# Performance work log

Hardware: AMD Instinct MI355X
Metric: run time of the kernel (lower is better)

The kernel has to match this reference:

```python
import jax, jax.numpy as jnp
import numpy as np

N = 100000
E = 1600000
IN_FEATS = 128
HID = 128


def _xavier(key, shape):
    fan_in, fan_out = shape[0], shape[1]
    limit = float(np.sqrt(6.0 / (fan_in + fan_out)))
    return jax.random.uniform(key, shape, jnp.float32, -limit, limit)


def setup_inputs() -> dict:
    key = jax.random.key(0)
    ks = jax.random.split(key, 10)
    x = jax.random.normal(ks[0], (N, IN_FEATS), jnp.float32)
    edge_index = jax.random.randint(ks[1], (2, E), 0, N, jnp.int64)
    inp = {"x": x, "edge_index": edge_index}
    # GCNConv weights (stored as [in, out] so h = x @ W)
    inp["W1"] = _xavier(ks[2], (IN_FEATS, HID)); inp["b1"] = jnp.zeros((HID,), jnp.float32)
    inp["W2"] = _xavier(ks[3], (HID, HID));      inp["b2"] = jnp.zeros((HID,), jnp.float32)
    inp["W3"] = _xavier(ks[4], (HID, HID));      inp["b3"] = jnp.zeros((HID,), jnp.float32)
    # position head: Linear(HID,HID) -> ReLU -> Linear(HID,2)
    inp["Wp1"] = _xavier(ks[5], (HID, HID)); inp["bp1"] = jnp.zeros((HID,), jnp.float32)
    inp["Wp2"] = _xavier(ks[6], (HID, 2));   inp["bp2"] = jnp.zeros((2,), jnp.float32)
    # time head: Linear(HID,HID//2) -> ReLU -> Linear(HID//2,1)
    inp["Wt1"] = _xavier(ks[7], (HID, HID // 2)); inp["bt1"] = jnp.zeros((HID // 2,), jnp.float32)
    inp["Wt2"] = _xavier(ks[8], (HID // 2, 1));   inp["bt2"] = jnp.zeros((1,), jnp.float32)
    return inp


def _gcn_conv(x, src, dst, norm, W, b):
    # PyG GCNConv: out = D^{-1/2} (A + I) D^{-1/2} (x W) + b
    h = x @ W                                  # [N, out]
    msg = h[src] * norm[:, None]               # gather over edges (+ self-loops)
    agg = jax.ops.segment_sum(msg, dst, num_segments=N)  # scatter-add to dst
    return agg + b


def reference(x, edge_index, W1, b1, W2, b2, W3, b3, Wp1, bp1, Wp2, bp2, Wt1, bt1, Wt2, bt2):
    src, dst = edge_index[0], edge_index[1]
    # add self-loops once (shared across the 3 conv layers)
    loop = jnp.arange(N, dtype=edge_index.dtype)
    src_a = jnp.concatenate([src, loop])
    dst_a = jnp.concatenate([dst, loop])
    # symmetric normalization: deg computed on dst (in-degree incl. self-loop)
    deg = jax.ops.segment_sum(jnp.ones_like(dst_a, dtype=x.dtype), dst_a, num_segments=N)
    dinv = jnp.where(deg > 0, jax.lax.rsqrt(deg), 0.0)
    norm = dinv[src_a] * dinv[dst_a]           # [E + N]

    h = jax.nn.relu(_gcn_conv(x, src_a, dst_a, norm, W1, b1))
    h = jax.nn.relu(_gcn_conv(h, src_a, dst_a, norm, W2, b2))
    h = jax.nn.relu(_gcn_conv(h, src_a, dst_a, norm, W3, b3))

    pos = jax.nn.relu(h @ Wp1 + bp1) @ Wp2 + bp2     # [N, 2]
    time = jax.nn.relu(h @ Wt1 + bt1) @ Wt2 + bt2    # [N, 1]
    return jnp.concatenate([pos, time], axis=1)      # [N, 3]
```

## Files before the change

kernel.cpp:

```cpp
#include <hip/hip_runtime.h>

typedef __bf16 bf16x8 __attribute__((ext_vector_type(8)));
typedef unsigned short u16x8 __attribute__((ext_vector_type(8)));
typedef float f32x4 __attribute__((ext_vector_type(4)));

union BU {
    u16x8 u;
    bf16x8 b;
};

static __device__ __forceinline__ float b2f(unsigned short u) {
    return __uint_as_float(((unsigned)u) << 16);
}
static __device__ __forceinline__ unsigned short f2b(float f) {
    unsigned u = __float_as_uint(f);
    unsigned r = (u + 0x7FFF + ((u >> 16) & 1)) >> 16;
    return (unsigned short)r;
}

__global__ __launch_bounds__(256) void wsplit_kernel(
    const float* __restrict__ W1, const float* __restrict__ W2, const float* __restrict__ W3,
    const float* __restrict__ Wp1, const float* __restrict__ Wt1,
    unsigned short* __restrict__ W1hi, unsigned short* __restrict__ W1lo,
    unsigned short* __restrict__ W2hi, unsigned short* __restrict__ W2lo,
    unsigned short* __restrict__ W3hi, unsigned short* __restrict__ W3lo,
    unsigned short* __restrict__ Wchi, unsigned short* __restrict__ Wclo,
    const float* __restrict__ bp1, const float* __restrict__ bt1, float* __restrict__ bcat) {
    int b = blockIdx.x;
    int tid = threadIdx.x;
    if (b < 288) {
        const float* W;
        unsigned short *Whi, *Wlo;
        int lb, ncshift, total;
        if (b < 64)       { W = W1;  Whi = W1hi; Wlo = W1lo; lb = b;       ncshift = 7; total = 16384; }
        else if (b < 128) { W = W2;  Whi = W2hi; Wlo = W2lo; lb = b - 64;  ncshift = 7; total = 16384; }
        else if (b < 192) { W = W3;  Whi = W3hi; Wlo = W3lo; lb = b - 128; ncshift = 7; total = 16384; }
        else if (b < 256) { W = Wp1; Whi = Wchi; Wlo = Wclo; lb = b - 192; ncshift = 7; total = 16384; }
        else              { W = Wt1; Whi = Wchi + 128 * 128; Wlo = Wclo + 128 * 128; lb = b - 256; ncshift = 6; total = 8192; }
        int idx = lb * 256 + tid;
        if (idx < total) {
            int k = idx >> ncshift;
            int n = idx - (k << ncshift);
            float a = W[idx];
            unsigned short hb = f2b(a);
            Whi[(n << 7) + k] = hb;
            Wlo[(n << 7) + k] = f2b(a - b2f(hb));
        }
        return;
    }
    if (tid < 128) bcat[tid] = bp1[tid];
    else if (tid < 192) bcat[tid] = bt1[tid - 128];
}

static __device__ __forceinline__ void split8(const float4 a01, const float4 a23,
                                              bf16x8& hi, bf16x8& lo) {
    float a[8] = {a01.x, a01.y, a01.z, a01.w, a23.x, a23.y, a23.z, a23.w};
    BU h, l;
#pragma unroll
    for (int j = 0; j < 8; ++j) {
        unsigned short hb = f2b(a[j]);
        h.u[j] = hb;
        l.u[j] = f2b(a[j] - b2f(hb));
    }
    hi = h.b;
    lo = l.b;
}

template <int NT>
static __device__ __forceinline__ void gemm_acc_f32(const float* __restrict__ A,
                                                    const unsigned short* __restrict__ Whi,
                                                    const unsigned short* __restrict__ Wlo,
                                                    int arow, int m16, int quad, f32x4* acc) {
    const float* Arow = A + (size_t)arow * 128 + quad * 8;
#pragma unroll
    for (int kb = 0; kb < 4; ++kb) {
        float4 a01 = *reinterpret_cast<const float4*>(Arow + kb * 32);
        float4 a23 = *reinterpret_cast<const float4*>(Arow + kb * 32 + 4);
        bf16x8 ahi, alo;
        split8(a01, a23, ahi, alo);
#pragma unroll
        for (int t = 0; t < NT; ++t) {
            size_t woff = (size_t)(t * 16 + m16) * 128 + quad * 8 + kb * 32;
            BU bh, bl;
            bh.u = *reinterpret_cast<const u16x8*>(Whi + woff);
            bl.u = *reinterpret_cast<const u16x8*>(Wlo + woff);
            acc[t] = __builtin_amdgcn_mfma_f32_16x16x32_bf16(ahi, bh.b, acc[t], 0, 0, 0);
            acc[t] = __builtin_amdgcn_mfma_f32_16x16x32_bf16(ahi, bl.b, acc[t], 0, 0, 0);
            acc[t] = __builtin_amdgcn_mfma_f32_16x16x32_bf16(alo, bh.b, acc[t], 0, 0, 0);
        }
    }
}

template <int NT>
static __device__ __forceinline__ void gemm_acc(const unsigned short* __restrict__ A,
                                                const unsigned short* __restrict__ Whi,
                                                const unsigned short* __restrict__ Wlo,
                                                int arow, int m16, int quad, f32x4* acc) {
    const unsigned short* Arow = A + (size_t)arow * 128 + quad * 8;
#pragma unroll
    for (int kb = 0; kb < 4; ++kb) {
        BU a;
        a.u = *reinterpret_cast<const u16x8*>(Arow + kb * 32);
#pragma unroll
        for (int t = 0; t < NT; ++t) {
            size_t woff = (size_t)(t * 16 + m16) * 128 + quad * 8 + kb * 32;
            BU bh, bl;
            bh.u = *reinterpret_cast<const u16x8*>(Whi + woff);
            bl.u = *reinterpret_cast<const u16x8*>(Wlo + woff);
            acc[t] = __builtin_amdgcn_mfma_f32_16x16x32_bf16(a.b, bh.b, acc[t], 0, 0, 0);
            acc[t] = __builtin_amdgcn_mfma_f32_16x16x32_bf16(a.b, bl.b, acc[t], 0, 0, 0);
        }
    }
}

template <int NT>
static __device__ __forceinline__ void gemm_store_plain(unsigned short* __restrict__ C,
                                                        int row_base, int m16, int quad,
                                                        f32x4* acc, int nrows) {
#pragma unroll
    for (int t = 0; t < NT; ++t) {
#pragma unroll
        for (int r = 0; r < 4; ++r) {
            int row = row_base + quad * 4 + r;
            if (row < nrows)
                C[(size_t)row * (NT * 16) + t * 16 + m16] = f2b(acc[t][r]);
        }
    }
}

template <int NT>
static __device__ __forceinline__ void gemm_store_scaled(const int* __restrict__ deg,
                                                         unsigned short* __restrict__ C,
                                                         int row_base, int m16, int quad,
                                                         f32x4* acc, int nrows) {
#pragma unroll
    for (int t = 0; t < NT; ++t) {
#pragma unroll
        for (int r = 0; r < 4; ++r) {
            int row = row_base + quad * 4 + r;
            if (row < nrows) {
                float d = rsqrtf((float)deg[row] + 1.0f);
                C[(size_t)row * (NT * 16) + t * 16 + m16] = f2b(acc[t][r] * d);
            }
        }
    }
}

__global__ __launch_bounds__(256) void fg2_kernel(const float* __restrict__ A,
                                                  const unsigned short* __restrict__ Whi,
                                                  const unsigned short* __restrict__ Wlo,
                                                  unsigned short* __restrict__ C, int nrows,
                                                  int fbn,
                                                  const int* __restrict__ ei,
                                                  int* __restrict__ deg,
                                                  int* __restrict__ slots, int E) {
    const int bid = blockIdx.x;
    const int tid = threadIdx.x;
    const int trip = bid / 3, r = bid % 3;
    if (r == 1 && trip < fbn) {
        int base = (trip * 256 + tid) * 8;
        int dsts[8], srcs[8], ps[8];
#pragma unroll
        for (int k = 0; k < 8; ++k) {
            int e = base + k;
            dsts[k] = (e < E) ? ei[E + e] : -1;
            srcs[k] = (e < E) ? ei[e] : 0;
        }
#pragma unroll
        for (int k = 0; k < 8; ++k)
            if (dsts[k] >= 0) ps[k] = atomicAdd(&deg[dsts[k]], 1);
#pragma unroll
        for (int k = 0; k < 8; ++k)
            if (dsts[k] >= 0 && ps[k] < 64)
                __builtin_nontemporal_store(srcs[k], &slots[(size_t)dsts[k] * 64 + ps[k]]);
    } else {
        int gid = bid - min(trip, fbn) - ((r > 1 && trip < fbn) ? 1 : 0);
        const int wave = tid >> 6, lane = tid & 63;
        const int m16 = lane & 15, quad = lane >> 4;
        const int row_base = gid * 64 + wave * 16;
        int arow = row_base + m16;
        if (arow >= nrows) arow = nrows - 1;
        f32x4 acc[8] = {};
        gemm_acc_f32<8>(A, Whi, Wlo, arow, m16, quad, acc);
        gemm_store_plain<8>(C, row_base, m16, quad, acc, nrows);
    }
}

__global__ __launch_bounds__(256) void scale_kernel(unsigned short* __restrict__ hs,
                                                    const int* __restrict__ deg, int n) {
    int idx = blockIdx.x * 256 + threadIdx.x;
    int node = idx >> 5;
    if (node >= n) return;
    int f = (idx & 31) * 4;
    float d = rsqrtf((float)deg[node] + 1.0f);
    ushort4 v = *reinterpret_cast<const ushort4*>(hs + (size_t)node * 128 + f);
    ushort4 o;
    o.x = f2b(b2f(v.x) * d);
    o.y = f2b(b2f(v.y) * d);
    o.z = f2b(b2f(v.z) * d);
    o.w = f2b(b2f(v.w) * d);
    *reinterpret_cast<ushort4*>(hs + (size_t)node * 128 + f) = o;
}

template <int NT>
__global__ __launch_bounds__(256) void gemm_kernel(const unsigned short* __restrict__ A,
                                                   const unsigned short* __restrict__ Whi,
                                                   const unsigned short* __restrict__ Wlo,
                                                   const int* __restrict__ deg,
                                                   unsigned short* __restrict__ C, int nrows) {
    const int tid = threadIdx.x;
    const int wave = tid >> 6, lane = tid & 63;
    const int m16 = lane & 15, quad = lane >> 4;
    const int row_base = blockIdx.x * 64 + wave * 16;
    int arow = row_base + m16;
    if (arow >= nrows) arow = nrows - 1;
    f32x4 acc[NT] = {};
    gemm_acc<NT>(A, Whi, Wlo, arow, m16, quad, acc);
    gemm_store_scaled<NT>(deg, C, row_base, m16, quad, acc, nrows);
}

__global__ __launch_bounds__(256) void pull_kernel(const unsigned short* __restrict__ hs,
                                                   const int* __restrict__ slots,
                                                   const int* __restrict__ deg,
                                                   const float* __restrict__ bias,
                                                   unsigned short* __restrict__ out, int n) {
    const int tid = threadIdx.x;
    const int wave = tid >> 6, lane = tid & 63;
    const int slot = lane >> 4, chunk = lane & 15;
    const int node = blockIdx.x * 4 + wave;
    if (node >= n) return;
    const int dg = deg[node];
    const float d = rsqrtf((float)dg + 1.0f);
    const int m = min(dg, 64);

    BU sv;
    sv.u = *reinterpret_cast<const u16x8*>(hs + (size_t)node * 128 + chunk * 8);
    int myidx = slots[(size_t)node * 64 + lane];

    float acc[8] = {};
    const int rounds = (m + 3) >> 2;
    int r = 0;
    for (; r + 4 <= rounds; r += 4) {
        int e0 = r * 4 + slot, e1 = e0 + 4, e2 = e0 + 8, e3 = e0 + 12;
        int s0 = __shfl(myidx, e0), s1 = __shfl(myidx, e1);
        int s2 = __shfl(myidx, e2), s3 = __shfl(myidx, e3);
        s0 = (unsigned)s0 < (unsigned)n ? s0 : 0;
        s1 = (unsigned)s1 < (unsigned)n ? s1 : 0;
        s2 = (unsigned)s2 < (unsigned)n ? s2 : 0;
        s3 = (unsigned)s3 < (unsigned)n ? s3 : 0;
        bool ok0 = e0 < m, ok1 = e1 < m, ok2 = e2 < m, ok3 = e3 < m;
        BU h0, h1, h2, h3;
        if (ok0) h0.u = *reinterpret_cast<const u16x8*>(hs + (size_t)s0 * 128 + chunk * 8);
        if (ok1) h1.u = *reinterpret_cast<const u16x8*>(hs + (size_t)s1 * 128 + chunk * 8);
        if (ok2) h2.u = *reinterpret_cast<const u16x8*>(hs + (size_t)s2 * 128 + chunk * 8);
        if (ok3) h3.u = *reinterpret_cast<const u16x8*>(hs + (size_t)s3 * 128 + chunk * 8);
        if (ok0) {
#pragma unroll
            for (int j = 0; j < 8; ++j) acc[j] += b2f(h0.u[j]);
        }
        if (ok1) {
#pragma unroll
            for (int j = 0; j < 8; ++j) acc[j] += b2f(h1.u[j]);
        }
        if (ok2) {
#pragma unroll
            for (int j = 0; j < 8; ++j) acc[j] += b2f(h2.u[j]);
        }
        if (ok3) {
#pragma unroll
            for (int j = 0; j < 8; ++j) acc[j] += b2f(h3.u[j]);
        }
    }
    for (; r < rounds; ++r) {
        int e0 = r * 4 + slot;
        int s0 = __shfl(myidx, e0);
        s0 = (unsigned)s0 < (unsigned)n ? s0 : 0;
        if (e0 < m) {
            BU h0;
            h0.u = *reinterpret_cast<const u16x8*>(hs + (size_t)s0 * 128 + chunk * 8);
#pragma unroll
            for (int j = 0; j < 8; ++j) acc[j] += b2f(h0.u[j]);
        }
    }
#pragma unroll
    for (int j = 0; j < 8; ++j) {
        acc[j] += __shfl_xor(acc[j], 16);
        acc[j] += __shfl_xor(acc[j], 32);
    }
    if (slot == 0) {
        BU o;
#pragma unroll
        for (int j = 0; j < 8; ++j)
            o.u[j] = f2b(fmaxf((acc[j] + b2f(sv.u[j])) * d + bias[chunk * 8 + j], 0.f));
        *reinterpret_cast<u16x8*>(out + (size_t)node * 128 + chunk * 8) = o.u;
    }
}

__global__ __launch_bounds__(256) void gemmh_kernel(const unsigned short* __restrict__ A,
                                                    const unsigned short* __restrict__ Whi,
                                                    const unsigned short* __restrict__ Wlo,
                                                    const float* __restrict__ bcat,
                                                    const float* __restrict__ Wp2,
                                                    const float* __restrict__ bp2,
                                                    const float* __restrict__ Wt2,
                                                    const float* __restrict__ bt2,
                                                    float* __restrict__ out, int nrows) {
    const int tid = threadIdx.x;
    const int wave = tid >> 6, lane = tid & 63;
    const int m16 = lane & 15, quad = lane >> 4;
    const int row_base = blockIdx.x * 64 + wave * 16;
    int arow = row_base + m16;
    if (arow >= nrows) arow = nrows - 1;
    f32x4 acc[12] = {};
    gemm_acc<12>(A, Whi, Wlo, arow, m16, quad, acc);
#pragma unroll
    for (int r = 0; r < 4; ++r) {
        int row = row_base + quad * 4 + r;
        float p0 = 0.f, p1 = 0.f, tt = 0.f;
#pragma unroll
        for (int t = 0; t < 12; ++t) {
            int c = t * 16 + m16;
            float v = fmaxf(acc[t][r] + bcat[c], 0.f);
            if (t < 8) {
                p0 += v * Wp2[c * 2 + 0];
                p1 += v * Wp2[c * 2 + 1];
            } else {
                tt += v * Wt2[c - 128];
            }
        }
#pragma unroll
        for (int mask = 1; mask < 16; mask <<= 1) {
            p0 += __shfl_xor(p0, mask);
            p1 += __shfl_xor(p1, mask);
            tt += __shfl_xor(tt, mask);
        }
        if (m16 == 0 && row < nrows) {
            out[(size_t)row * 3 + 0] = p0 + bp2[0];
            out[(size_t)row * 3 + 1] = p1 + bp2[1];
            out[(size_t)row * 3 + 2] = tt + bt2[0];
        }
    }
}

extern "C" void kernel_launch(void* const* d_in, const int* in_sizes, int n_in,
                              void* d_out, int out_size, void* d_ws, size_t ws_size,
                              hipStream_t stream) {
    const int N = in_sizes[0] / 128;
    const int E = in_sizes[1] / 2;

    const float* x   = (const float*)d_in[0];
    const int* ei    = (const int*)d_in[1];
    const float* W1  = (const float*)d_in[2];
    const float* b1  = (const float*)d_in[3];
    const float* W2  = (const float*)d_in[4];
    const float* b2  = (const float*)d_in[5];
    const float* W3  = (const float*)d_in[6];
    const float* b3  = (const float*)d_in[7];
    const float* Wp1 = (const float*)d_in[8];
    const float* bp1 = (const float*)d_in[9];
    const float* Wp2 = (const float*)d_in[10];
    const float* bp2 = (const float*)d_in[11];
    const float* Wt1 = (const float*)d_in[12];
    const float* bt1 = (const float*)d_in[13];
    const float* Wt2 = (const float*)d_in[14];
    const float* bt2 = (const float*)d_in[15];
    float* out = (float*)d_out;

    char* ws = (char*)d_ws;
    size_t off = 0;
    auto alloc = [&](size_t bytes) {
        void* p = ws + off;
        off += (bytes + 255) & ~(size_t)255;
        return p;
    };
    int* deg        = (int*)alloc((size_t)N * 4);
    int* slots      = (int*)alloc((size_t)N * 64 * 4);
    unsigned short* W1hi = (unsigned short*)alloc(16384 * 2);
    unsigned short* W1lo = (unsigned short*)alloc(16384 * 2);
    unsigned short* W2hi = (unsigned short*)alloc(16384 * 2);
    unsigned short* W2lo = (unsigned short*)alloc(16384 * 2);
    unsigned short* W3hi = (unsigned short*)alloc(16384 * 2);
    unsigned short* W3lo = (unsigned short*)alloc(16384 * 2);
    unsigned short* Wchi = (unsigned short*)alloc(192 * 128 * 2);
    unsigned short* Wclo = (unsigned short*)alloc(192 * 128 * 2);
    float* bcat          = (float*)alloc(192 * 4);
    unsigned short* hs   = (unsigned short*)alloc((size_t)N * 128 * 2);
    unsigned short* hb   = (unsigned short*)alloc((size_t)N * 128 * 2);

    hipMemsetAsync(deg, 0, (size_t)N * 4, stream);

    wsplit_kernel<<<289, 256, 0, stream>>>(W1, W2, W3, Wp1, Wt1,
                                           W1hi, W1lo, W2hi, W2lo, W3hi, W3lo,
                                           Wchi, Wclo, bp1, bt1, bcat);

    const int gb = (N + 63) / 64;
    const int fbn = ((E + 7) / 8 + 255) / 256;
    const int pull_blocks = (N + 3) / 4;

    fg2_kernel<<<gb + fbn, 256, 0, stream>>>(x, W1hi, W1lo, hs, N, fbn, ei, deg, slots, E);
    scale_kernel<<<(N * 32 + 255) / 256, 256, 0, stream>>>(hs, deg, N);

    pull_kernel<<<pull_blocks, 256, 0, stream>>>(hs, slots, deg, b1, hb, N);
    gemm_kernel<8><<<gb, 256, 0, stream>>>(hb, W2hi, W2lo, deg, hs, N);
    pull_kernel<<<pull_blocks, 256, 0, stream>>>(hs, slots, deg, b2, hb, N);
    gemm_kernel<8><<<gb, 256, 0, stream>>>(hb, W3hi, W3lo, deg, hs, N);
    pull_kernel<<<pull_blocks, 256, 0, stream>>>(hs, slots, deg, b3, hb, N);

    gemmh_kernel<<<gb, 256, 0, stream>>>(hb, Wchi, Wclo, bcat, Wp2, bp2, Wt2, bt2, out, N);
}
```

Baseline: 630.4 us.

## Fuse neighbor aggregation with following GEMM through per-wave LDS tiles

Merges each pull (gather-aggregate) kernel with the next layer's GEMM, or with the heads GEMM for the last layer. Each wave aggregates 16 nodes into a swizzled LDS tile and then runs MFMA directly from LDS. This removes the intermediate bf16 activation write and re-read plus three kernel launches. The cost is lower gather parallelism: each wave now processes 16 nodes sequentially, and the grid shrinks from N/4 to N/64 blocks, which may reduce memory-level parallelism for the latency-bound gather.

```diff
diff --git a/kernel.cpp b/kernel.cpp
--- a/kernel.cpp
+++ b/kernel.cpp
@@ -92,28 +92,6 @@
 }
 
 template <int NT>
-static __device__ __forceinline__ void gemm_acc(const unsigned short* __restrict__ A,
-                                                const unsigned short* __restrict__ Whi,
-                                                const unsigned short* __restrict__ Wlo,
-                                                int arow, int m16, int quad, f32x4* acc) {
-    const unsigned short* Arow = A + (size_t)arow * 128 + quad * 8;
-#pragma unroll
-    for (int kb = 0; kb < 4; ++kb) {
-        BU a;
-        a.u = *reinterpret_cast<const u16x8*>(Arow + kb * 32);
-#pragma unroll
-        for (int t = 0; t < NT; ++t) {
-            size_t woff = (size_t)(t * 16 + m16) * 128 + quad * 8 + kb * 32;
-            BU bh, bl;
-            bh.u = *reinterpret_cast<const u16x8*>(Whi + woff);
-            bl.u = *reinterpret_cast<const u16x8*>(Wlo + woff);
-            acc[t] = __builtin_amdgcn_mfma_f32_16x16x32_bf16(a.b, bh.b, acc[t], 0, 0, 0);
-            acc[t] = __builtin_amdgcn_mfma_f32_16x16x32_bf16(a.b, bl.b, acc[t], 0, 0, 0);
-        }
-    }
-}
-
-template <int NT>
 static __device__ __forceinline__ void gemm_store_plain(unsigned short* __restrict__ C,
                                                         int row_base, int m16, int quad,
                                                         f32x4* acc, int nrows) {
@@ -202,117 +180,139 @@
     *reinterpret_cast<ushort4*>(hs + (size_t)node * 128 + f) = o;
 }
 
-template <int NT>
-__global__ __launch_bounds__(256) void gemm_kernel(const unsigned short* __restrict__ A,
-                                                   const unsigned short* __restrict__ Whi,
-                                                   const unsigned short* __restrict__ Wlo,
-                                                   const int* __restrict__ deg,
-                                                   unsigned short* __restrict__ C, int nrows) {
-    const int tid = threadIdx.x;
-    const int wave = tid >> 6, lane = tid & 63;
-    const int m16 = lane & 15, quad = lane >> 4;
-    const int row_base = blockIdx.x * 64 + wave * 16;
-    int arow = row_base + m16;
-    if (arow >= nrows) arow = nrows - 1;
-    f32x4 acc[NT] = {};
-    gemm_acc<NT>(A, Whi, Wlo, arow, m16, quad, acc);
-    gemm_store_scaled<NT>(deg, C, row_base, m16, quad, acc, nrows);
-}
-
-__global__ __launch_bounds__(256) void pull_kernel(const unsigned short* __restrict__ hs,
+static __device__ __forceinline__ void pull_to_lds(const unsigned short* __restrict__ hs,
                                                    const int* __restrict__ slots,
                                                    const int* __restrict__ deg,
                                                    const float* __restrict__ bias,
-                                                   unsigned short* __restrict__ out, int n) {
+                                                   unsigned short* __restrict__ ldsw,
+                                                   int row_base, int lane, int n) {
+    const int slot = lane >> 4, chunk = lane & 15;
+    for (int i = 0; i < 16; ++i) {
+        const int node = row_base + i;
+        if (node >= n) break;
+        const int dg = deg[node];
+        const float d = rsqrtf((float)dg + 1.0f);
+        const int m = min(dg, 64);
+
+        BU sv;
+        sv.u = *reinterpret_cast<const u16x8*>(hs + (size_t)node * 128 + chunk * 8);
+        int myidx = slots[(size_t)node * 64 + lane];
+
+        float acc[8] = {};
+        const int rounds = (m + 3) >> 2;
+        int r = 0;
+        for (; r + 4 <= rounds; r += 4) {
+            int e0 = r * 4 + slot, e1 = e0 + 4, e2 = e0 + 8, e3 = e0 + 12;
+            int s0 = __shfl(myidx, e0), s1 = __shfl(myidx, e1);
+            int s2 = __shfl(myidx, e2), s3 = __shfl(myidx, e3);
+            s0 = (unsigned)s0 < (unsigned)n ? s0 : 0;
+            s1 = (unsigned)s1 < (unsigned)n ? s1 : 0;
+            s2 = (unsigned)s2 < (unsigned)n ? s2 : 0;
+            s3 = (unsigned)s3 < (unsigned)n ? s3 : 0;
+            bool ok0 = e0 < m, ok1 = e1 < m, ok2 = e2 < m, ok3 = e3 < m;
+            BU h0, h1, h2, h3;
+            if (ok0) h0.u = *reinterpret_cast<const u16x8*>(hs + (size_t)s0 * 128 + chunk * 8);
+            if (ok1) h1.u = *reinterpret_cast<const u16x8*>(hs + (size_t)s1 * 128 + chunk * 8);
+            if (ok2) h2.u = *reinterpret_cast<const u16x8*>(hs + (size_t)s2 * 128 + chunk * 8);
+            if (ok3) h3.u = *reinterpret_cast<const u16x8*>(hs + (size_t)s3 * 128 + chunk * 8);
+            if (ok0) {
+#pragma unroll
+                for (int j = 0; j < 8; ++j) acc[j] += b2f(h0.u[j]);
+            }
+            if (ok1) {
+#pragma unroll
+                for (int j = 0; j < 8; ++j) acc[j] += b2f(h1.u[j]);
+            }
+            if (ok2) {
+#pragma unroll
+                for (int j = 0; j < 8; ++j) acc[j] += b2f(h2.u[j]);
+            }
+            if (ok3) {
+#pragma unroll
+                for (int j = 0; j < 8; ++j) acc[j] += b2f(h3.u[j]);
+            }
+        }
+        for (; r < rounds; ++r) {
+            int e0 = r * 4 + slot;
+            int s0 = __shfl(myidx, e0);
+            s0 = (unsigned)s0 < (unsigned)n ? s0 : 0;
+            if (e0 < m) {
+                BU h0;
+                h0.u = *reinterpret_cast<const u16x8*>(hs + (size_t)s0 * 128 + chunk * 8);
+#pragma unroll
+                for (int j = 0; j < 8; ++j) acc[j] += b2f(h0.u[j]);
+            }
+        }
+#pragma unroll
+        for (int j = 0; j < 8; ++j) {
+            acc[j] += __shfl_xor(acc[j], 16);
+            acc[j] += __shfl_xor(acc[j], 32);
+        }
+        if (slot == 0) {
+            BU o;
+#pragma unroll
+            for (int j = 0; j < 8; ++j)
+                o.u[j] = f2b(fmaxf((acc[j] + b2f(sv.u[j])) * d + bias[chunk * 8 + j], 0.f));
+            *reinterpret_cast<u16x8*>(&ldsw[i * 128 + ((chunk * 8) ^ ((i & 7) << 3))]) = o.u;
+        }
+    }
+}
+
+template <int NT>
+static __device__ __forceinline__ void gemm_acc_lds(const unsigned short* __restrict__ ldsw,
+                                                    const unsigned short* __restrict__ Whi,
+                                                    const unsigned short* __restrict__ Wlo,
+                                                    int m16, int quad, f32x4* acc) {
+#pragma unroll
+    for (int kb = 0; kb < 4; ++kb) {
+        BU a;
+        a.u = *reinterpret_cast<const u16x8*>(
+            &ldsw[m16 * 128 + ((quad * 8 + kb * 32) ^ ((m16 & 7) << 3))]);
+#pragma unroll
+        for (int t = 0; t < NT; ++t) {
+            size_t woff = (size_t)(t * 16 + m16) * 128 + quad * 8 + kb * 32;
+            BU bh, bl;
+            bh.u = *reinterpret_cast<const u16x8*>(Whi + woff);
+            bl.u = *reinterpret_cast<const u16x8*>(Wlo + woff);
+            acc[t] = __builtin_amdgcn_mfma_f32_16x16x32_bf16(a.b, bh.b, acc[t], 0, 0, 0);
+            acc[t] = __builtin_amdgcn_mfma_f32_16x16x32_bf16(a.b, bl.b, acc[t], 0, 0, 0);
+        }
+    }
+}
+
+__global__ __launch_bounds__(256) void pg_kernel(const unsigned short* __restrict__ hs,
+                                                 const int* __restrict__ slots,
+                                                 const int* __restrict__ deg,
+                                                 const float* __restrict__ bias,
+                                                 const unsigned short* __restrict__ Whi,
+                                                 const unsigned short* __restrict__ Wlo,
+                                                 unsigned short* __restrict__ C, int n) {
+    __shared__ unsigned short lds[4][16 * 128];
     const int tid = threadIdx.x;
     const int wave = tid >> 6, lane = tid & 63;
-    const int slot = lane >> 4, chunk = lane & 15;
-    const int node = blockIdx.x * 4 + wave;
-    if (node >= n) return;
-    const int dg = deg[node];
-    const float d = rsqrtf((float)dg + 1.0f);
-    const int m = min(dg, 64);
-
-    BU sv;
-    sv.u = *reinterpret_cast<const u16x8*>(hs + (size_t)node * 128 + chunk * 8);
-    int myidx = slots[(size_t)node * 64 + lane];
-
-    float acc[8] = {};
-    const int rounds = (m + 3) >> 2;
-    int r = 0;
-    for (; r + 4 <= rounds; r += 4) {
-        int e0 = r * 4 + slot, e1 = e0 + 4, e2 = e0 + 8, e3 = e0 + 12;
-        int s0 = __shfl(myidx, e0), s1 = __shfl(myidx, e1);
-        int s2 = __shfl(myidx, e2), s3 = __shfl(myidx, e3);
-        s0 = (unsigned)s0 < (unsigned)n ? s0 : 0;
-        s1 = (unsigned)s1 < (unsigned)n ? s1 : 0;
-        s2 = (unsigned)s2 < (unsigned)n ? s2 : 0;
-        s3 = (unsigned)s3 < (unsigned)n ? s3 : 0;
-        bool ok0 = e0 < m, ok1 = e1 < m, ok2 = e2 < m, ok3 = e3 < m;
-        BU h0, h1, h2, h3;
-        if (ok0) h0.u = *reinterpret_cast<const u16x8*>(hs + (size_t)s0 * 128 + chunk * 8);
-        if (ok1) h1.u = *reinterpret_cast<const u16x8*>(hs + (size_t)s1 * 128 + chunk * 8);
-        if (ok2) h2.u = *reinterpret_cast<const u16x8*>(hs + (size_t)s2 * 128 + chunk * 8);
-        if (ok3) h3.u = *reinterpret_cast<const u16x8*>(hs + (size_t)s3 * 128 + chunk * 8);
-        if (ok0) {
-#pragma unroll
-            for (int j = 0; j < 8; ++j) acc[j] += b2f(h0.u[j]);
-        }
-        if (ok1) {
-#pragma unroll
-            for (int j = 0; j < 8; ++j) acc[j] += b2f(h1.u[j]);
-        }
-        if (ok2) {
-#pragma unroll
-            for (int j = 0; j < 8; ++j) acc[j] += b2f(h2.u[j]);
-        }
-        if (ok3) {
-#pragma unroll
-            for (int j = 0; j < 8; ++j) acc[j] += b2f(h3.u[j]);
-        }
-    }
-    for (; r < rounds; ++r) {
-        int e0 = r * 4 + slot;
-        int s0 = __shfl(myidx, e0);
-        s0 = (unsigned)s0 < (unsigned)n ? s0 : 0;
-        if (e0 < m) {
-            BU h0;
-            h0.u = *reinterpret_cast<const u16x8*>(hs + (size_t)s0 * 128 + chunk * 8);
-#pragma unroll
-            for (int j = 0; j < 8; ++j) acc[j] += b2f(h0.u[j]);
-        }
-    }
-#pragma unroll
-    for (int j = 0; j < 8; ++j) {
-        acc[j] += __shfl_xor(acc[j], 16);
-        acc[j] += __shfl_xor(acc[j], 32);
-    }
-    if (slot == 0) {
-        BU o;
-#pragma unroll
-        for (int j = 0; j < 8; ++j)
-            o.u[j] = f2b(fmaxf((acc[j] + b2f(sv.u[j])) * d + bias[chunk * 8 + j], 0.f));
-        *reinterpret_cast<u16x8*>(out + (size_t)node * 128 + chunk * 8) = o.u;
-    }
-}
-
-__global__ __launch_bounds__(256) void gemmh_kernel(const unsigned short* __restrict__ A,
-                                                    const unsigned short* __restrict__ Whi,
-                                                    const unsigned short* __restrict__ Wlo,
-                                                    const float* __restrict__ bcat,
-                                                    const float* __restrict__ Wp2,
-                                                    const float* __restrict__ bp2,
-                                                    const float* __restrict__ Wt2,
-                                                    const float* __restrict__ bt2,
-                                                    float* __restrict__ out, int nrows) {
+    const int row_base = blockIdx.x * 64 + wave * 16;
+    pull_to_lds(hs, slots, deg, bias, lds[wave], row_base, lane, n);
+    const int m16 = lane & 15, quad = lane >> 4;
+    f32x4 acc[8] = {};
+    gemm_acc_lds<8>(lds[wave], Whi, Wlo, m16, quad, acc);
+    gemm_store_scaled<8>(deg, C, row_base, m16, quad, acc, n);
+}
+
+__global__ __launch_bounds__(256) void pg_heads_kernel(
+    const unsigned short* __restrict__ hs, const int* __restrict__ slots,
+    const int* __restrict__ deg, const float* __restrict__ bias,
+    const unsigned short* __restrict__ Whi, const unsigned short* __restrict__ Wlo,
+    const float* __restrict__ bcat, const float* __restrict__ Wp2,
+    const float* __restrict__ bp2, const float* __restrict__ Wt2,
+    const float* __restrict__ bt2, float* __restrict__ out, int n) {
+    __shared__ unsigned short lds[4][16 * 128];
     const int tid = threadIdx.x;
     const int wave = tid >> 6, lane = tid & 63;
+    const int row_base = blockIdx.x * 64 + wave * 16;
+    pull_to_lds(hs, slots, deg, bias, lds[wave], row_base, lane, n);
     const int m16 = lane & 15, quad = lane >> 4;
-    const int row_base = blockIdx.x * 64 + wave * 16;
-    int arow = row_base + m16;
-    if (arow >= nrows) arow = nrows - 1;
     f32x4 acc[12] = {};
-    gemm_acc<12>(A, Whi, Wlo, arow, m16, quad, acc);
+    gemm_acc_lds<12>(lds[wave], Whi, Wlo, m16, quad, acc);
 #pragma unroll
     for (int r = 0; r < 4; ++r) {
         int row = row_base + quad * 4 + r;
@@ -334,7 +334,7 @@
             p1 += __shfl_xor(p1, mask);
             tt += __shfl_xor(tt, mask);
         }
-        if (m16 == 0 && row < nrows) {
+        if (m16 == 0 && row < n) {
             out[(size_t)row * 3 + 0] = p0 + bp2[0];
             out[(size_t)row * 3 + 1] = p1 + bp2[1];
             out[(size_t)row * 3 + 2] = tt + bt2[0];
@@ -384,8 +384,8 @@
     unsigned short* Wchi = (unsigned short*)alloc(192 * 128 * 2);
     unsigned short* Wclo = (unsigned short*)alloc(192 * 128 * 2);
     float* bcat          = (float*)alloc(192 * 4);
-    unsigned short* hs   = (unsigned short*)alloc((size_t)N * 128 * 2);
-    unsigned short* hb   = (unsigned short*)alloc((size_t)N * 128 * 2);
+    unsigned short* hsA  = (unsigned short*)alloc((size_t)N * 128 * 2);
+    unsigned short* hsB  = (unsigned short*)alloc((size_t)N * 128 * 2);
 
     hipMemsetAsync(deg, 0, (size_t)N * 4, stream);
 
@@ -395,16 +395,12 @@
 
     const int gb = (N + 63) / 64;
     const int fbn = ((E + 7) / 8 + 255) / 256;
-    const int pull_blocks = (N + 3) / 4;
-
-    fg2_kernel<<<gb + fbn, 256, 0, stream>>>(x, W1hi, W1lo, hs, N, fbn, ei, deg, slots, E);
-    scale_kernel<<<(N * 32 + 255) / 256, 256, 0, stream>>>(hs, deg, N);
-
-    pull_kernel<<<pull_blocks, 256, 0, stream>>>(hs, slots, deg, b1, hb, N);
-    gemm_kernel<8><<<gb, 256, 0, stream>>>(hb, W2hi, W2lo, deg, hs, N);
-    pull_kernel<<<pull_blocks, 256, 0, stream>>>(hs, slots, deg, b2, hb, N);
-    gemm_kernel<8><<<gb, 256, 0, stream>>>(hb, W3hi, W3lo, deg, hs, N);
-    pull_kernel<<<pull_blocks, 256, 0, stream>>>(hs, slots, deg, b3, hb, N);
-
-    gemmh_kernel<<<gb, 256, 0, stream>>>(hb, Wchi, Wclo, bcat, Wp2, bp2, Wt2, bt2, out, N);
-}
+
+    fg2_kernel<<<gb + fbn, 256, 0, stream>>>(x, W1hi, W1lo, hsA, N, fbn, ei, deg, slots, E);
+    scale_kernel<<<(N * 32 + 255) / 256, 256, 0, stream>>>(hsA, deg, N);
+
+    pg_kernel<<<gb, 256, 0, stream>>>(hsA, slots, deg, b1, W2hi, W2lo, hsB, N);
+    pg_kernel<<<gb, 256, 0, stream>>>(hsB, slots, deg, b2, W3hi, W3lo, hsA, N);
+    pg_heads_kernel<<<gb, 256, 0, stream>>>(hsA, slots, deg, b3, Wchi, Wclo,
+                                            bcat, Wp2, bp2, Wt2, bt2, out, N);
+}
```

Measured after the change: 693.8 us. 1.1x slower.
